# Performance work log

Measured on AMD Instinct MI355X. Metric: run time of the kernel, lower is better.

Reference implementation:

```python
import jax, jax.numpy as jnp
import numpy as np

EMB_DIM = 1024
NUM_HEADS = 16
HEAD_DIM = EMB_DIM // NUM_HEADS


def setup_inputs() -> dict:
    key = jax.random.key(0)
    ks = jax.random.split(key, 6)
    B, T, D = 4, 2048, EMB_DIM
    s = 1.0 / np.sqrt(D)
    return {
        "x": jax.random.normal(ks[0], (B, T, D), dtype=jnp.float32),
        "Wq": jax.random.normal(ks[1], (D, D), dtype=jnp.float32) * s,
        "Wk": jax.random.normal(ks[2], (D, D), dtype=jnp.float32) * s,
        "Wv": jax.random.normal(ks[3], (D, D), dtype=jnp.float32) * s,
        "Wo": jax.random.normal(ks[4], (D, D), dtype=jnp.float32) * s,
        "bo": jax.random.normal(ks[5], (D,), dtype=jnp.float32) * 0.01,
    }


def reference(x, Wq, Wk, Wv, Wo, bo):
    B, T, D = x.shape
    H, Hd = NUM_HEADS, HEAD_DIM
    # Linear projections (torch Linear: x @ W.T); weights here stored as [in, out]
    q = (x @ Wq).reshape(B, T, H, Hd).transpose(0, 2, 1, 3)  # [B,H,T,Hd]
    k = (x @ Wk).reshape(B, T, H, Hd).transpose(0, 2, 1, 3)
    v = (x @ Wv).reshape(B, T, H, Hd).transpose(0, 2, 1, 3)
    scores = jnp.einsum("bhqd,bhkd->bhqk", q, k) / jnp.sqrt(jnp.float32(Hd))
    causal = jnp.tril(jnp.ones((T, T), dtype=bool))
    scores = jnp.where(causal, scores, -jnp.inf)
    weights = jax.nn.softmax(scores, axis=-1)  # drop_rate=0 -> dropout is identity
    ctx = jnp.einsum("bhqk,bhkd->bhqd", weights, v)
    ctx = ctx.transpose(0, 2, 1, 3).reshape(B, T, D)
    return ctx @ Wo + bo
```

## Files before the change

kernel.cpp:

```cpp
#include <hip/hip_runtime.h>
#include <hip/hip_bf16.h>
#include <math.h>

#define TSEQ   2048
#define BATCH  4
#define DIM    1024
#define NH     16
#define HD     64
#define MTOT   (BATCH*TSEQ)

typedef __attribute__((ext_vector_type(8))) short bf16x8;
typedef __attribute__((ext_vector_type(4))) float f32x4;

__device__ __forceinline__ unsigned short f2bf(float f) {
    unsigned int b = __float_as_uint(f);
    b = (b + 0x7fffu + ((b >> 16) & 1u)) >> 16;
    return (unsigned short)b;
}

__global__ __launch_bounds__(256)
void cvt_x(const float* __restrict__ in, unsigned short* __restrict__ out, int n8)
{
    int i = blockIdx.x * 256 + threadIdx.x;
    if (i >= n8) return;
    const float4* p = (const float4*)in + 2 * (size_t)i;
    float4 a = p[0], b = p[1];
    bf16x8 o;
    o[0] = (short)f2bf(a.x); o[1] = (short)f2bf(a.y);
    o[2] = (short)f2bf(a.z); o[3] = (short)f2bf(a.w);
    o[4] = (short)f2bf(b.x); o[5] = (short)f2bf(b.y);
    o[6] = (short)f2bf(b.z); o[7] = (short)f2bf(b.w);
    *((bf16x8*)out + i) = o;
}

__global__ __launch_bounds__(256)
void cvt_tr(const float* __restrict__ W, unsigned short* __restrict__ WT)
{
    __shared__ float t[32][33];
    const int x = threadIdx.x, y0 = threadIdx.y;
    const int bx = blockIdx.x, by = blockIdx.y;
#pragma unroll
    for (int j = 0; j < 4; ++j)
        t[y0 + j*8][x] = W[(size_t)(by*32 + y0 + j*8) * DIM + bx*32 + x];
    __syncthreads();
#pragma unroll
    for (int j = 0; j < 4; ++j)
        WT[(size_t)(bx*32 + y0 + j*8) * DIM + by*32 + x] = f2bf(t[x][y0 + j*8]);
}

template<bool F32OUT>
__global__ __launch_bounds__(256)
void gemm_bf16(const unsigned short* __restrict__ A, const unsigned short* __restrict__ BT,
               const float* __restrict__ bias, void* __restrict__ Cout,
               const int M, const int N, const int K)
{
    __shared__ unsigned short As[128*32];
    __shared__ unsigned short Bs[128*32];
    const int t = threadIdx.x;
    const int w = t >> 6, lane = t & 63, g = lane >> 4, li = lane & 15;
    const int wm = (w >> 1) * 64, wn = (w & 1) * 64;
    const int m0 = blockIdx.x * 128, n0 = blockIdx.y * 128;

    f32x4 acc[4][4] = {};

    const int r0 = t >> 1, c0 = (t & 1) * 2;
    const unsigned short* Ap = &A [(size_t)(m0 + r0) * K + c0*8];
    const unsigned short* Bp = &BT[(size_t)(n0 + r0) * K + c0*8];
    char* AsB = (char*)As;
    char* BsB = (char*)Bs;
    const int sw  = (r0 >> 1) & 3;
    const int wa0 = r0*64 + ((c0       ^ sw) * 16);
    const int wa1 = r0*64 + (((c0 + 1) ^ sw) * 16);

    for (int kt = 0; kt < K; kt += 32) {
        bf16x8 a0 = *(const bf16x8*)(Ap + kt);
        bf16x8 a1 = *(const bf16x8*)(Ap + kt + 8);
        bf16x8 b0 = *(const bf16x8*)(Bp + kt);
        bf16x8 b1 = *(const bf16x8*)(Bp + kt + 8);
        __syncthreads();
        *(bf16x8*)(AsB + wa0) = a0;
        *(bf16x8*)(AsB + wa1) = a1;
        *(bf16x8*)(BsB + wa0) = b0;
        *(bf16x8*)(BsB + wa1) = b1;
        __syncthreads();

        bf16x8 af[4], bfv[4];
#pragma unroll
        for (int mi = 0; mi < 4; ++mi) {
            const int r = wm + mi*16 + li;
            af[mi] = *(const bf16x8*)(AsB + r*64 + ((g ^ ((r >> 1) & 3)) * 16));
        }
#pragma unroll
        for (int ni = 0; ni < 4; ++ni) {
            const int r = wn + ni*16 + li;
            bfv[ni] = *(const bf16x8*)(BsB + r*64 + ((g ^ ((r >> 1) & 3)) * 16));
        }
#pragma unroll
        for (int mi = 0; mi < 4; ++mi)
#pragma unroll
            for (int ni = 0; ni < 4; ++ni)
                acc[mi][ni] = __builtin_amdgcn_mfma_f32_16x16x32_bf16(
                    af[mi], bfv[ni], acc[mi][ni], 0, 0, 0);
    }

#pragma unroll
    for (int mi = 0; mi < 4; ++mi)
#pragma unroll
        for (int ni = 0; ni < 4; ++ni) {
            const int gr = m0 + wm + mi*16 + 4*g;
            const int gc = n0 + wn + ni*16 + li;
#pragma unroll
            for (int r = 0; r < 4; ++r) {
                const float v = acc[mi][ni][r];
                if (F32OUT)
                    ((float*)Cout)[(size_t)(gr + r) * N + gc] = v + bias[gc];
                else
                    ((unsigned short*)Cout)[(size_t)(gr + r) * N + gc] = f2bf(v);
            }
        }
}

__global__ __launch_bounds__(256)
void attn_bf16(const unsigned short* __restrict__ Q, const unsigned short* __restrict__ Km,
               const unsigned short* __restrict__ V, unsigned short* __restrict__ O)
{
    __shared__ unsigned short Ks[64*64];
    __shared__ unsigned short VT[64*64];
    __shared__ unsigned short Ps[64*64];
    const int t = threadIdx.x;
    const int w = t >> 6, lane = t & 63, g = lane >> 4, li = lane & 15;
    const int qt = (int)gridDim.x - 1 - (int)blockIdx.x;
    const int bh = blockIdx.y, b = bh >> 4, h = bh & 15;
    const int q0 = qt * 64;
    const size_t rowbase = (size_t)b * TSEQ;
    const int cb = h * HD;

    bf16x8 qa[2];
#pragma unroll
    for (int ks = 0; ks < 2; ++ks)
        qa[ks] = *(const bf16x8*)&Q[(rowbase + q0 + w*16 + li) * DIM + cb + 8*g + 32*ks];

    f32x4 ctx[4] = {};
    float m_i[4], l_i[4];
#pragma unroll
    for (int r = 0; r < 4; ++r) { m_i[r] = -INFINITY; l_i[r] = 0.f; }

    char* KsB = (char*)Ks;
    char* VTB = (char*)VT;
    char* PsB = (char*)Ps;

    for (int kv = 0; kv <= qt; ++kv) {
        __syncthreads();
        const size_t kbase = rowbase + kv*64;
#pragma unroll
        for (int i = 0; i < 2; ++i) {
            const int tc = 2*t + i;
            const int r = tc >> 3, c = tc & 7;
            bf16x8 kk = *(const bf16x8*)&Km[(kbase + r) * DIM + cb + c*8];
            *(bf16x8*)(KsB + r*128 + ((c ^ (r & 7)) * 16)) = kk;
        }
        const int kvr = t & 63;
#pragma unroll
        for (int i = 0; i < 2; ++i) {
            const int dc = (t >> 6) * 2 + i;
            bf16x8 vv = *(const bf16x8*)&V[(kbase + kvr) * DIM + cb + dc*8];
#pragma unroll
            for (int j = 0; j < 8; ++j) {
                const int d = dc*8 + j;
                *(unsigned short*)(VTB + d*128 + (((kvr >> 3) ^ (d & 7)) * 16)
                                   + (kvr & 7) * 2) = (unsigned short)vv[j];
            }
        }
        __syncthreads();

        f32x4 s[4] = {};
#pragma unroll
        for (int nt = 0; nt < 4; ++nt) {
            const int r = nt*16 + li;
#pragma unroll
            for (int ks = 0; ks < 2; ++ks) {
                bf16x8 kb = *(const bf16x8*)(KsB + r*128 + (((g + 4*ks) ^ (r & 7)) * 16));
                s[nt] = __builtin_amdgcn_mfma_f32_16x16x32_bf16(qa[ks], kb, s[nt], 0, 0, 0);
            }
        }
#pragma unroll
        for (int nt = 0; nt < 4; ++nt) s[nt] *= 0.125f;
        if (kv == qt) {
#pragma unroll
            for (int nt = 0; nt < 4; ++nt) {
                const int kvl = nt*16 + li;
#pragma unroll
                for (int r = 0; r < 4; ++r)
                    if (kvl > w*16 + 4*g + r) s[nt][r] = -INFINITY;
            }
        }

#pragma unroll
        for (int r = 0; r < 4; ++r) {
            float mx = fmaxf(fmaxf(s[0][r], s[1][r]), fmaxf(s[2][r], s[3][r]));
            mx = fmaxf(mx, __shfl_xor(mx, 1));
            mx = fmaxf(mx, __shfl_xor(mx, 2));
            mx = fmaxf(mx, __shfl_xor(mx, 4));
            mx = fmaxf(mx, __shfl_xor(mx, 8));
            const float mnew = fmaxf(m_i[r], mx);
            const float sc = __expf(m_i[r] - mnew);
            const float p0 = __expf(s[0][r] - mnew), p1 = __expf(s[1][r] - mnew);
            const float p2 = __expf(s[2][r] - mnew), p3 = __expf(s[3][r] - mnew);
            float rs = p0 + p1 + p2 + p3;
            rs += __shfl_xor(rs, 1);
            rs += __shfl_xor(rs, 2);
            rs += __shfl_xor(rs, 4);
            rs += __shfl_xor(rs, 8);
            l_i[r] = l_i[r]*sc + rs;
            m_i[r] = mnew;
#pragma unroll
            for (int n2 = 0; n2 < 4; ++n2) ctx[n2][r] *= sc;
            const int q = w*16 + 4*g + r;
            const int ch = li >> 3, cl = (li & 7)*2, qs = q & 7;
            *(unsigned short*)(PsB + q*128 + (((0 + ch) ^ qs)*16) + cl) = f2bf(p0);
            *(unsigned short*)(PsB + q*128 + (((2 + ch) ^ qs)*16) + cl) = f2bf(p1);
            *(unsigned short*)(PsB + q*128 + (((4 + ch) ^ qs)*16) + cl) = f2bf(p2);
            *(unsigned short*)(PsB + q*128 + (((6 + ch) ^ qs)*16) + cl) = f2bf(p3);
        }

        bf16x8 pa[2];
#pragma unroll
        for (int ks = 0; ks < 2; ++ks) {
            const int r = w*16 + li;
            pa[ks] = *(const bf16x8*)(PsB + r*128 + (((g + 4*ks) ^ (r & 7)) * 16));
        }
#pragma unroll
        for (int n2 = 0; n2 < 4; ++n2) {
            const int r = n2*16 + li;
#pragma unroll
            for (int ks = 0; ks < 2; ++ks) {
                bf16x8 vb = *(const bf16x8*)(VTB + r*128 + (((g + 4*ks) ^ (r & 7)) * 16));
                ctx[n2] = __builtin_amdgcn_mfma_f32_16x16x32_bf16(pa[ks], vb, ctx[n2], 0, 0, 0);
            }
        }
    }

#pragma unroll
    for (int r = 0; r < 4; ++r) {
        const float inv = 1.f / l_i[r];
        const size_t row = rowbase + q0 + w*16 + 4*g + r;
#pragma unroll
        for (int n2 = 0; n2 < 4; ++n2)
            O[row * DIM + cb + n2*16 + li] = f2bf(ctx[n2][r] * inv);
    }
}

extern "C" void kernel_launch(void* const* d_in, const int* in_sizes, int n_in,
                              void* d_out, int out_size, void* d_ws, size_t ws_size,
                              hipStream_t stream)
{
    const float* x  = (const float*)d_in[0];
    const float* Wq = (const float*)d_in[1];
    const float* Wk = (const float*)d_in[2];
    const float* Wv = (const float*)d_in[3];
    const float* Wo = (const float*)d_in[4];
    const float* bo = (const float*)d_in[5];
    float* out = (float*)d_out;

    char* ws = (char*)d_ws;
    unsigned short* xb  = (unsigned short*)(ws);
    unsigned short* qb  = (unsigned short*)(ws + (16u << 20));
    unsigned short* kb  = (unsigned short*)(ws + (32u << 20));
    unsigned short* vb  = (unsigned short*)(ws + (48u << 20));
    unsigned short* ctb = (unsigned short*)(ws + (64u << 20));
    unsigned short* WqT = (unsigned short*)(ws + (80u << 20));
    unsigned short* WkT = (unsigned short*)(ws + (82u << 20));
    unsigned short* WvT = (unsigned short*)(ws + (84u << 20));
    unsigned short* WoT = (unsigned short*)(ws + (86u << 20));

    cvt_x<<<MTOT*DIM/8/256, 256, 0, stream>>>(x, xb, MTOT*DIM/8);
    dim3 tb(32, 8), tg(32, 32);
    cvt_tr<<<tg, tb, 0, stream>>>(Wq, WqT);
    cvt_tr<<<tg, tb, 0, stream>>>(Wk, WkT);
    cvt_tr<<<tg, tb, 0, stream>>>(Wv, WvT);
    cvt_tr<<<tg, tb, 0, stream>>>(Wo, WoT);

    dim3 gg(MTOT/128, DIM/128);
    gemm_bf16<false><<<gg, 256, 0, stream>>>(xb, WqT, nullptr, qb, MTOT, DIM, DIM);
    gemm_bf16<false><<<gg, 256, 0, stream>>>(xb, WkT, nullptr, kb, MTOT, DIM, DIM);
    gemm_bf16<false><<<gg, 256, 0, stream>>>(xb, WvT, nullptr, vb, MTOT, DIM, DIM);

    attn_bf16<<<dim3(TSEQ/64, BATCH*NH), 256, 0, stream>>>(qb, kb, vb, ctb);

    gemm_bf16<true><<<gg, 256, 0, stream>>>(ctb, WoT, bo, out, MTOT, DIM, DIM);
}
```

Measured before the change: 450.8 us.

## Fuse QKV GEMMs, use direct-to-LDS loads, double-buffer attention K/V

Concatenates the Q/K/V weight transposes and runs a single N=3072 projection GEMM writing an interleaved QKV buffer, removing two launches and rereads of x. The GEMM tile staging switches to global_load_lds so data goes straight to shared memory without passing through registers. The attention kernel double-buffers K and V tiles, prefetching the next block during compute, and drops one barrier per iteration. Softmax switches to exp2 with a prescaled log2e factor and only rescales the running max when it grows by more than 8, which trades exact max tracking for fewer rescales but adds some risk of overflow or precision loss.

Result: slower. 543.1 us (+20.5%).

```diff
diff --git a/kernel.cpp b/kernel.cpp
--- a/kernel.cpp
+++ b/kernel.cpp
@@ -8,6 +8,7 @@
 #define NH     16
 #define HD     64
 #define MTOT   (BATCH*TSEQ)
+#define LDQKV  (3*DIM)
 
 typedef __attribute__((ext_vector_type(8))) short bf16x8;
 typedef __attribute__((ext_vector_type(4))) float f32x4;
@@ -16,6 +17,12 @@
     unsigned int b = __float_as_uint(f);
     b = (b + 0x7fffu + ((b >> 16) & 1u)) >> 16;
     return (unsigned short)b;
+}
+
+__device__ __forceinline__ void glds16(const void* g, void* l) {
+    __builtin_amdgcn_global_load_lds(
+        (const __attribute__((address_space(1))) void*)g,
+        (__attribute__((address_space(3))) void*)l, 16, 0, 0);
 }
 
 __global__ __launch_bounds__(256)
@@ -50,7 +57,7 @@
 
 template<bool F32OUT>
 __global__ __launch_bounds__(256)
-void gemm_bf16(const unsigned short* __restrict__ A, const unsigned short* __restrict__ BT,
+void gemm_glds(const unsigned short* __restrict__ A, const unsigned short* __restrict__ BT,
                const float* __restrict__ bias, void* __restrict__ Cout,
                const int M, const int N, const int K)
 {
@@ -63,25 +70,30 @@
 
     f32x4 acc[4][4] = {};
 
-    const int r0 = t >> 1, c0 = (t & 1) * 2;
-    const unsigned short* Ap = &A [(size_t)(m0 + r0) * K + c0*8];
-    const unsigned short* Bp = &BT[(size_t)(n0 + r0) * K + c0*8];
+    const int r_a  = w*32 + (lane >> 2);
+    const int r_b  = r_a + 16;
+    const int slot = lane & 3;
+    const int sc0  = slot ^ ((r_a >> 1) & 3);
+    const int sc1  = slot ^ ((r_b >> 1) & 3);
+
+    const unsigned short* Ap0 = &A [(size_t)(m0 + r_a) * K + sc0*8];
+    const unsigned short* Ap1 = &A [(size_t)(m0 + r_b) * K + sc1*8];
+    const unsigned short* Bp0 = &BT[(size_t)(n0 + r_a) * K + sc0*8];
+    const unsigned short* Bp1 = &BT[(size_t)(n0 + r_b) * K + sc1*8];
+    unsigned short* AsW0 = &As[w*1024];
+    unsigned short* AsW1 = &As[w*1024 + 512];
+    unsigned short* BsW0 = &Bs[w*1024];
+    unsigned short* BsW1 = &Bs[w*1024 + 512];
+
     char* AsB = (char*)As;
     char* BsB = (char*)Bs;
-    const int sw  = (r0 >> 1) & 3;
-    const int wa0 = r0*64 + ((c0       ^ sw) * 16);
-    const int wa1 = r0*64 + (((c0 + 1) ^ sw) * 16);
 
     for (int kt = 0; kt < K; kt += 32) {
-        bf16x8 a0 = *(const bf16x8*)(Ap + kt);
-        bf16x8 a1 = *(const bf16x8*)(Ap + kt + 8);
-        bf16x8 b0 = *(const bf16x8*)(Bp + kt);
-        bf16x8 b1 = *(const bf16x8*)(Bp + kt + 8);
         __syncthreads();
-        *(bf16x8*)(AsB + wa0) = a0;
-        *(bf16x8*)(AsB + wa1) = a1;
-        *(bf16x8*)(BsB + wa0) = b0;
-        *(bf16x8*)(BsB + wa1) = b1;
+        glds16(Ap0 + kt, AsW0);
+        glds16(Ap1 + kt, AsW1);
+        glds16(Bp0 + kt, BsW0);
+        glds16(Bp1 + kt, BsW1);
         __syncthreads();
 
         bf16x8 af[4], bfv[4];
@@ -120,12 +132,13 @@
         }
 }
 
+#define SCL2E 0.18033688f
+
 __global__ __launch_bounds__(256)
-void attn_bf16(const unsigned short* __restrict__ Q, const unsigned short* __restrict__ Km,
-               const unsigned short* __restrict__ V, unsigned short* __restrict__ O)
-{
-    __shared__ unsigned short Ks[64*64];
-    __shared__ unsigned short VT[64*64];
+void attn_bf16(const unsigned short* __restrict__ QKV, unsigned short* __restrict__ O)
+{
+    __shared__ unsigned short Ks[2][64*64];
+    __shared__ unsigned short VT[2][64*64];
     __shared__ unsigned short Ps[64*64];
     const int t = threadIdx.x;
     const int w = t >> 6, lane = t & 63, g = lane >> 4, li = lane & 15;
@@ -133,45 +146,55 @@
     const int bh = blockIdx.y, b = bh >> 4, h = bh & 15;
     const int q0 = qt * 64;
     const size_t rowbase = (size_t)b * TSEQ;
-    const int cb = h * HD;
+    const int cq = h*HD, ck = DIM + h*HD, cv = 2*DIM + h*HD;
 
     bf16x8 qa[2];
 #pragma unroll
     for (int ks = 0; ks < 2; ++ks)
-        qa[ks] = *(const bf16x8*)&Q[(rowbase + q0 + w*16 + li) * DIM + cb + 8*g + 32*ks];
+        qa[ks] = *(const bf16x8*)&QKV[(rowbase + q0 + w*16 + li) * LDQKV + cq + 8*g + 32*ks];
 
     f32x4 ctx[4] = {};
     float m_i[4], l_i[4];
 #pragma unroll
     for (int r = 0; r < 4; ++r) { m_i[r] = -INFINITY; l_i[r] = 0.f; }
 
-    char* KsB = (char*)Ks;
-    char* VTB = (char*)VT;
     char* PsB = (char*)Ps;
 
+    const int krow   = lane >> 3;
+    const int kchunk = (lane & 7) ^ krow;
+    const int kr0 = 16*w + krow, kr1 = 16*w + 8 + krow;
+    const int kvr = t & 63;
+    const int dc0 = 2*w, dc1 = 2*w + 1;
+
+    {
+        const size_t nb = rowbase;
+        glds16(&QKV[(nb + kr0) * LDQKV + ck + kchunk*8], &Ks[0][(2*w    )*512]);
+        glds16(&QKV[(nb + kr1) * LDQKV + ck + kchunk*8], &Ks[0][(2*w + 1)*512]);
+        bf16x8 v0 = *(const bf16x8*)&QKV[(nb + kvr) * LDQKV + cv + dc0*8];
+        bf16x8 v1 = *(const bf16x8*)&QKV[(nb + kvr) * LDQKV + cv + dc1*8];
+        char* VTB = (char*)VT[0];
+#pragma unroll
+        for (int j = 0; j < 8; ++j) {
+            const int d0 = dc0*8 + j, d1 = dc1*8 + j;
+            *(unsigned short*)(VTB + d0*128 + (((kvr >> 3) ^ (d0 & 7)) * 16) + (kvr & 7)*2) = (unsigned short)v0[j];
+            *(unsigned short*)(VTB + d1*128 + (((kvr >> 3) ^ (d1 & 7)) * 16) + (kvr & 7)*2) = (unsigned short)v1[j];
+        }
+    }
+    __syncthreads();
+
+    int cur = 0;
     for (int kv = 0; kv <= qt; ++kv) {
-        __syncthreads();
-        const size_t kbase = rowbase + kv*64;
-#pragma unroll
-        for (int i = 0; i < 2; ++i) {
-            const int tc = 2*t + i;
-            const int r = tc >> 3, c = tc & 7;
-            bf16x8 kk = *(const bf16x8*)&Km[(kbase + r) * DIM + cb + c*8];
-            *(bf16x8*)(KsB + r*128 + ((c ^ (r & 7)) * 16)) = kk;
-        }
-        const int kvr = t & 63;
-#pragma unroll
-        for (int i = 0; i < 2; ++i) {
-            const int dc = (t >> 6) * 2 + i;
-            bf16x8 vv = *(const bf16x8*)&V[(kbase + kvr) * DIM + cb + dc*8];
-#pragma unroll
-            for (int j = 0; j < 8; ++j) {
-                const int d = dc*8 + j;
-                *(unsigned short*)(VTB + d*128 + (((kvr >> 3) ^ (d & 7)) * 16)
-                                   + (kvr & 7) * 2) = (unsigned short)vv[j];
-            }
-        }
-        __syncthreads();
+        bf16x8 vn0, vn1;
+        if (kv < qt) {
+            const size_t nb = rowbase + (size_t)(kv + 1) * 64;
+            glds16(&QKV[(nb + kr0) * LDQKV + ck + kchunk*8], &Ks[cur^1][(2*w    )*512]);
+            glds16(&QKV[(nb + kr1) * LDQKV + ck + kchunk*8], &Ks[cur^1][(2*w + 1)*512]);
+            vn0 = *(const bf16x8*)&QKV[(nb + kvr) * LDQKV + cv + dc0*8];
+            vn1 = *(const bf16x8*)&QKV[(nb + kvr) * LDQKV + cv + dc1*8];
+        }
+
+        char* KsB = (char*)Ks[cur];
+        char* VTB = (char*)VT[cur];
 
         f32x4 s[4] = {};
 #pragma unroll
@@ -184,7 +207,7 @@
             }
         }
 #pragma unroll
-        for (int nt = 0; nt < 4; ++nt) s[nt] *= 0.125f;
+        for (int nt = 0; nt < 4; ++nt) s[nt] *= SCL2E;
         if (kv == qt) {
 #pragma unroll
             for (int nt = 0; nt < 4; ++nt) {
@@ -202,19 +225,21 @@
             mx = fmaxf(mx, __shfl_xor(mx, 2));
             mx = fmaxf(mx, __shfl_xor(mx, 4));
             mx = fmaxf(mx, __shfl_xor(mx, 8));
-            const float mnew = fmaxf(m_i[r], mx);
-            const float sc = __expf(m_i[r] - mnew);
-            const float p0 = __expf(s[0][r] - mnew), p1 = __expf(s[1][r] - mnew);
-            const float p2 = __expf(s[2][r] - mnew), p3 = __expf(s[3][r] - mnew);
+            if (mx > m_i[r] + 8.f) {
+                const float sc = exp2f(m_i[r] - mx);
+                m_i[r] = mx;
+                l_i[r] *= sc;
+#pragma unroll
+                for (int n2 = 0; n2 < 4; ++n2) ctx[n2][r] *= sc;
+            }
+            const float p0 = exp2f(s[0][r] - m_i[r]), p1 = exp2f(s[1][r] - m_i[r]);
+            const float p2 = exp2f(s[2][r] - m_i[r]), p3 = exp2f(s[3][r] - m_i[r]);
             float rs = p0 + p1 + p2 + p3;
             rs += __shfl_xor(rs, 1);
             rs += __shfl_xor(rs, 2);
             rs += __shfl_xor(rs, 4);
             rs += __shfl_xor(rs, 8);
-            l_i[r] = l_i[r]*sc + rs;
-            m_i[r] = mnew;
-#pragma unroll
-            for (int n2 = 0; n2 < 4; ++n2) ctx[n2][r] *= sc;
+            l_i[r] += rs;
             const int q = w*16 + 4*g + r;
             const int ch = li >> 3, cl = (li & 7)*2, qs = q & 7;
             *(unsigned short*)(PsB + q*128 + (((0 + ch) ^ qs)*16) + cl) = f2bf(p0);
@@ -238,6 +263,18 @@
                 ctx[n2] = __builtin_amdgcn_mfma_f32_16x16x32_bf16(pa[ks], vb, ctx[n2], 0, 0, 0);
             }
         }
+
+        if (kv < qt) {
+            char* VTN = (char*)VT[cur^1];
+#pragma unroll
+            for (int j = 0; j < 8; ++j) {
+                const int d0 = dc0*8 + j, d1 = dc1*8 + j;
+                *(unsigned short*)(VTN + d0*128 + (((kvr >> 3) ^ (d0 & 7)) * 16) + (kvr & 7)*2) = (unsigned short)vn0[j];
+                *(unsigned short*)(VTN + d1*128 + (((kvr >> 3) ^ (d1 & 7)) * 16) + (kvr & 7)*2) = (unsigned short)vn1[j];
+            }
+            __syncthreads();
+            cur ^= 1;
+        }
     }
 
 #pragma unroll
@@ -246,7 +283,7 @@
         const size_t row = rowbase + q0 + w*16 + 4*g + r;
 #pragma unroll
         for (int n2 = 0; n2 < 4; ++n2)
-            O[row * DIM + cb + n2*16 + li] = f2bf(ctx[n2][r] * inv);
+            O[row * DIM + h*HD + n2*16 + li] = f2bf(ctx[n2][r] * inv);
     }
 }
 
@@ -263,29 +300,24 @@
     float* out = (float*)d_out;
 
     char* ws = (char*)d_ws;
-    unsigned short* xb  = (unsigned short*)(ws);
-    unsigned short* qb  = (unsigned short*)(ws + (16u << 20));
-    unsigned short* kb  = (unsigned short*)(ws + (32u << 20));
-    unsigned short* vb  = (unsigned short*)(ws + (48u << 20));
-    unsigned short* ctb = (unsigned short*)(ws + (64u << 20));
-    unsigned short* WqT = (unsigned short*)(ws + (80u << 20));
-    unsigned short* WkT = (unsigned short*)(ws + (82u << 20));
-    unsigned short* WvT = (unsigned short*)(ws + (84u << 20));
-    unsigned short* WoT = (unsigned short*)(ws + (86u << 20));
+    unsigned short* xb    = (unsigned short*)(ws);
+    unsigned short* qkv   = (unsigned short*)(ws + (16u << 20));
+    unsigned short* ctb   = (unsigned short*)(ws + (64u << 20));
+    unsigned short* WTall = (unsigned short*)(ws + (80u << 20));
+    unsigned short* WoT   = (unsigned short*)(ws + (86u << 20));
 
     cvt_x<<<MTOT*DIM/8/256, 256, 0, stream>>>(x, xb, MTOT*DIM/8);
     dim3 tb(32, 8), tg(32, 32);
-    cvt_tr<<<tg, tb, 0, stream>>>(Wq, WqT);
-    cvt_tr<<<tg, tb, 0, stream>>>(Wk, WkT);
-    cvt_tr<<<tg, tb, 0, stream>>>(Wv, WvT);
+    cvt_tr<<<tg, tb, 0, stream>>>(Wq, WTall);
+    cvt_tr<<<tg, tb, 0, stream>>>(Wk, WTall + (size_t)DIM*DIM);
+    cvt_tr<<<tg, tb, 0, stream>>>(Wv, WTall + (size_t)2*DIM*DIM);
     cvt_tr<<<tg, tb, 0, stream>>>(Wo, WoT);
 
-    dim3 gg(MTOT/128, DIM/128);
-    gemm_bf16<false><<<gg, 256, 0, stream>>>(xb, WqT, nullptr, qb, MTOT, DIM, DIM);
-    gemm_bf16<false><<<gg, 256, 0, stream>>>(xb, WkT, nullptr, kb, MTOT, DIM, DIM);
-    gemm_bf16<false><<<gg, 256, 0, stream>>>(xb, WvT, nullptr, vb, MTOT, DIM, DIM);
-
-    attn_bf16<<<dim3(TSEQ/64, BATCH*NH), 256, 0, stream>>>(qb, kb, vb, ctb);
-
-    gemm_bf16<true><<<gg, 256, 0, stream>>>(ctb, WoT, bo, out, MTOT, DIM, DIM);
-}
+    gemm_glds<false><<<dim3(MTOT/128, LDQKV/128), 256, 0, stream>>>(
+        xb, WTall, nullptr, qkv, MTOT, LDQKV, DIM);
+
+    attn_bf16<<<dim3(TSEQ/64, BATCH*NH), 256, 0, stream>>>(qkv, ctb);
+
+    gemm_glds<true><<<dim3(MTOT/128, DIM/128), 256, 0, stream>>>(
+        ctb, WoT, bo, out, MTOT, DIM, DIM);
+}
```
